# Performance work log

Measured on AMD Instinct MI355X. Metric: run time of the kernel, lower is better.

Reference implementation:

```python
import jax, jax.numpy as jnp
import numpy as np

N_HEAD = 16
ROPE_BASE = 10000.0


def _rotate_half(x):
    # interleaved rotate: (-x2, x1) pairs, matching torch stack+flatten
    x1 = x[..., ::2]
    x2 = x[..., 1::2]
    return jnp.stack((-x2, x1), axis=-1).reshape(x.shape)


def setup_inputs() -> dict:
    key = jax.random.key(0)
    ks = jax.random.split(key, 5)
    B, S, C = 4, 2048, 1024
    sc = 1.0 / np.sqrt(C)
    return {
        "x": jax.random.normal(ks[0], (B, S, C), jnp.float32),
        "W_qkv": jax.random.normal(ks[1], (C, 3 * C), jnp.float32) * sc,
        "b_qkv": jax.random.normal(ks[2], (3 * C,), jnp.float32) * 0.02,
        "W_proj": jax.random.normal(ks[3], (C, C), jnp.float32) * sc,
        "b_proj": jax.random.normal(ks[4], (C,), jnp.float32) * 0.02,
    }


def reference(x, W_qkv, b_qkv, W_proj, b_proj):
    B, S, C = x.shape
    H = N_HEAD
    D = C // H

    qkv = x @ W_qkv + b_qkv                       # [B,S,3C]
    q, k, v = jnp.split(qkv, 3, axis=-1)
    q = q.reshape(B, S, H, D).transpose(0, 2, 1, 3)  # [B,H,S,D]
    k = k.reshape(B, S, H, D).transpose(0, 2, 1, 3)
    v = v.reshape(B, S, H, D).transpose(0, 2, 1, 3)

    # RoPE cache (offset=0), faithful to source: emb = cat(freqs, freqs)
    inv_freq = 1.0 / (ROPE_BASE ** (jnp.arange(0, D, 2, dtype=jnp.float32) / D))
    pos = jnp.arange(S, dtype=jnp.float32)
    freqs = jnp.outer(pos, inv_freq)              # [S, D/2]
    emb = jnp.concatenate((freqs, freqs), axis=-1)  # [S, D]
    cos = jnp.cos(emb)[None, None, :, :]
    sin = jnp.sin(emb)[None, None, :, :]

    q = q * cos + _rotate_half(q) * sin
    k = k * cos + _rotate_half(k) * sin

    scale = 1.0 / jnp.sqrt(jnp.asarray(D, x.dtype))
    scores = jnp.einsum("bhqd,bhkd->bhqk", q, k) * scale  # [B,H,S,S]
    causal = jnp.tril(jnp.ones((S, S), dtype=bool))
    scores = jnp.where(causal[None, None], scores, jnp.asarray(-jnp.inf, x.dtype))
    att = jax.nn.softmax(scores, axis=-1)
    out = jnp.einsum("bhqk,bhkd->bhqd", att, v)    # [B,H,S,D]

    out = out.transpose(0, 2, 1, 3).reshape(B, S, C)
    out = out @ W_proj + b_proj                    # dropout=0 (eval)
    return out
```

## Files before the change

### kernel.cpp

```cpp
#include <hip/hip_runtime.h>
#include <hip/hip_bf16.h>
#include <math.h>

#define B_ 4
#define S_ 2048
#define C_ 1024
#define H_ 16
#define D_ 64
#define M_ (B_*S_)
#define NQKV (3*C_)
#define KDIM C_

typedef float f32x4 __attribute__((ext_vector_type(4)));
typedef float f32x16 __attribute__((ext_vector_type(16)));
typedef short bf16x8 __attribute__((ext_vector_type(8)));

static __device__ __forceinline__ ushort f2bf(float f){
    __hip_bfloat16 h = __float2bfloat16(f);
    union { __hip_bfloat16 b; ushort u; } v; v.b = h;
    return v.u;
}

static __device__ __forceinline__ void gload16(const ushort* g, ushort* l){
    __builtin_amdgcn_global_load_lds((__attribute__((address_space(1))) void*)g,
                                     (__attribute__((address_space(3))) void*)l,
                                     16, 0, 0);
}

__global__ void k_prep(const float* __restrict__ x, const float* __restrict__ Wqkv,
                       const float* __restrict__ Wproj,
                       ushort* __restrict__ xb, ushort* __restrict__ wqt,
                       ushort* __restrict__ wpt, unsigned* __restrict__ csT){
    __shared__ float tile[32][33];
    int blk = blockIdx.x, tid = threadIdx.x;
    if (blk < 2048){
        const int n4 = M_*KDIM/4;
        for (int i = blk*256 + tid; i < n4; i += 2048*256){
            float4 v = *(const float4*)(x + (size_t)i*4);
            ushort4 o = { f2bf(v.x), f2bf(v.y), f2bf(v.z), f2bf(v.w) };
            *(ushort4*)(xb + (size_t)i*4) = o;
        }
    } else if (blk < 5120){
        int t = blk - 2048;
        int c0 = (t % 96)*32, r0 = (t / 96)*32;
        int tx = tid & 31, ty = tid >> 5;
        for (int j = ty; j < 32; j += 8)
            tile[j][tx] = Wqkv[(size_t)(r0 + j)*NQKV + c0 + tx];
        __syncthreads();
        for (int j = ty; j < 32; j += 8)
            wqt[(size_t)(c0 + tx)*KDIM + r0 + j] = f2bf(tile[j][tx]);
    } else if (blk < 6144){
        int t = blk - 5120;
        int c0 = (t & 31)*32, r0 = (t >> 5)*32;
        int tx = tid & 31, ty = tid >> 5;
        for (int j = ty; j < 32; j += 8)
            tile[j][tx] = Wproj[(size_t)(r0 + j)*C_ + c0 + tx];
        __syncthreads();
        for (int j = ty; j < 32; j += 8)
            wpt[(size_t)(c0 + tx)*KDIM + r0 + j] = f2bf(tile[j][tx]);
    } else {
        int t = (blk - 6144)*256 + tid;
        int d = t >> 11, pos = t & 2047;
        float invf = powf(10000.0f, -(float)(d & 31) / 32.0f);
        float ang = (float)pos * invf;
        csT[t] = (unsigned)f2bf(cosf(ang)) | ((unsigned)f2bf(sinf(ang)) << 16);
    }
}

__launch_bounds__(512, 4)
__global__ void k_qkv(const ushort* __restrict__ xb, const ushort* __restrict__ wt,
                      const float* __restrict__ bqkv, const unsigned* __restrict__ csT,
                      ushort* __restrict__ qb, ushort* __restrict__ kb, ushort* __restrict__ vT){
    __shared__ __align__(16) ushort As[2][256][32];
    __shared__ __align__(16) ushort Bs[2][128][32];
    int bid = blockIdx.x;
    int lin = (bid & 7)*96 + (bid >> 3);
    int bx = lin % 24, by = lin / 24;
    int M0 = by*256, N0 = bx*128;
    int tid = threadIdx.x;
    int wid = tid >> 6, lane = tid & 63;
    int wm = wid >> 1, wn = wid & 1;
    int lrow = lane & 15, lk = lane >> 4;
    int swu = (lrow >> 1) & 3;

    int scol = (((lane & 3) ^ ((lane >> 3) & 3))) * 8;
    const ushort* gA0 = &xb[(size_t)(M0 + wid*16 + (lane >> 2))*KDIM + scol];
    const ushort* gA1 = gA0 + (size_t)128*KDIM;
    const ushort* gB0 = &wt[(size_t)(N0 + wid*16 + (lane >> 2))*KDIM + scol];

    f32x4 acc[4][4] = {};
    int cur = 0;
    gload16(gA0, &As[0][wid*16][0]);
    gload16(gA1, &As[0][128 + wid*16][0]);
    gload16(gB0, &Bs[0][wid*16][0]);
    __syncthreads();

    for (int k0 = 0; k0 < KDIM; k0 += 32){
        int nk = k0 + 32;
        if (nk < KDIM){
            gload16(gA0 + nk, &As[cur^1][wid*16][0]);
            gload16(gA1 + nk, &As[cur^1][128 + wid*16][0]);
            gload16(gB0 + nk, &Bs[cur^1][wid*16][0]);
        }
        bf16x8 a[4], b[4];
#pragma unroll
        for (int mi = 0; mi < 4; mi++)
            a[mi] = *(const bf16x8*)(&As[cur][wm*64 + mi*16 + lrow][(lk ^ swu)*8]);
#pragma unroll
        for (int ni = 0; ni < 4; ni++)
            b[ni] = *(const bf16x8*)(&Bs[cur][wn*64 + ni*16 + lrow][(lk ^ swu)*8]);
#pragma unroll
        for (int mi = 0; mi < 4; mi++)
#pragma unroll
            for (int ni = 0; ni < 4; ni++)
                acc[mi][ni] = __builtin_amdgcn_mfma_f32_16x16x32_bf16(a[mi], b[ni], acc[mi][ni], 0, 0, 0);
        __syncthreads();
        cur ^= 1;
    }
#pragma unroll
    for (int mi = 0; mi < 4; mi++)
#pragma unroll
    for (int ni = 0; ni < 4; ni++){
        int gn = N0 + wn*64 + ni*16 + lrow;
        float bias = bqkv[gn];
        int which = gn >> 10;
        int cn = gn & 1023;
        int h = cn >> 6, d = cn & 63;
        int gm0 = M0 + wm*64 + mi*16 + lk*4;
        int bb = gm0 >> 11, pos0 = gm0 & 2047;
        if (which == 2){
            ushort4 o = { f2bf(acc[mi][ni][0] + bias), f2bf(acc[mi][ni][1] + bias),
                          f2bf(acc[mi][ni][2] + bias), f2bf(acc[mi][ni][3] + bias) };
            *(ushort4*)(&vT[(((size_t)(bb*H_ + h))*D_ + d)*S_ + pos0]) = o;
        } else {
            uint4 cs4 = *(const uint4*)(&csT[d*2048 + pos0]);
            unsigned csa[4] = { cs4.x, cs4.y, cs4.z, cs4.w };
#pragma unroll
            for (int rr = 0; rr < 4; rr++){
                float val = acc[mi][ni][rr] + bias;
                float rot = __shfl_xor(val, 1);
                unsigned cs = csa[rr];
                float c = __uint_as_float(cs << 16);
                float s = __uint_as_float(cs & 0xffff0000u);
                float o = val*c + ((d & 1) ? rot : -rot)*s;
                if (which == 0) o *= 0.18033688f;
                int out_idx = (((bb*H_ + h)*S_) + pos0 + rr)*D_ + d;
                ((which == 0) ? qb : kb)[out_idx] = f2bf(o);
            }
        }
    }
}

__launch_bounds__(512, 4)
__global__ void k_proj(const ushort* __restrict__ ab, const ushort* __restrict__ wt,
                       const float* __restrict__ bias, float* __restrict__ out){
    __shared__ __align__(16) ushort As[2][256][32];
    __shared__ __align__(16) ushort Bs[2][128][32];
    int bid = blockIdx.x;
    int lin = (bid & 7)*32 + (bid >> 3);
    int bx = lin & 7, by = lin >> 3;
    int M0 = by*256, N0 = bx*128;
    int tid = threadIdx.x;
    int wid = tid >> 6, lane = tid & 63;
    int wm = wid >> 1, wn = wid & 1;
    int lrow = lane & 15, lk = lane >> 4;
    int swu = (lrow >> 1) & 3;

    int scol = (((lane & 3) ^ ((lane >> 3) & 3))) * 8;
    const ushort* gA0 = &ab[(size_t)(M0 + wid*16 + (lane >> 2))*KDIM + scol];
    const ushort* gA1 = gA0 + (size_t)128*KDIM;
    const ushort* gB0 = &wt[(size_t)(N0 + wid*16 + (lane >> 2))*KDIM + scol];

    f32x4 acc[4][4] = {};
    int cur = 0;
    gload16(gA0, &As[0][wid*16][0]);
    gload16(gA1, &As[0][128 + wid*16][0]);
    gload16(gB0, &Bs[0][wid*16][0]);
    __syncthreads();

    for (int k0 = 0; k0 < KDIM; k0 += 32){
        int nk = k0 + 32;
        if (nk < KDIM){
            gload16(gA0 + nk, &As[cur^1][wid*16][0]);
            gload16(gA1 + nk, &As[cur^1][128 + wid*16][0]);
            gload16(gB0 + nk, &Bs[cur^1][wid*16][0]);
        }
        bf16x8 a[4], b[4];
#pragma unroll
        for (int mi = 0; mi < 4; mi++)
            a[mi] = *(const bf16x8*)(&As[cur][wm*64 + mi*16 + lrow][(lk ^ swu)*8]);
#pragma unroll
        for (int ni = 0; ni < 4; ni++)
            b[ni] = *(const bf16x8*)(&Bs[cur][wn*64 + ni*16 + lrow][(lk ^ swu)*8]);
#pragma unroll
        for (int mi = 0; mi < 4; mi++)
#pragma unroll
            for (int ni = 0; ni < 4; ni++)
                acc[mi][ni] = __builtin_amdgcn_mfma_f32_16x16x32_bf16(a[mi], b[ni], acc[mi][ni], 0, 0, 0);
        __syncthreads();
        cur ^= 1;
    }
#pragma unroll
    for (int mi = 0; mi < 4; mi++)
#pragma unroll
    for (int ni = 0; ni < 4; ni++){
        int gn = N0 + wn*64 + ni*16 + lrow;
        float bv = bias[gn];
#pragma unroll
        for (int rr = 0; rr < 4; rr++){
            int gm = M0 + wm*64 + mi*16 + lk*4 + rr;
            out[(size_t)gm*C_ + gn] = acc[mi][ni][rr] + bv;
        }
    }
}

__launch_bounds__(256, 3)
__global__ void k_attn(const ushort* __restrict__ qb, const ushort* __restrict__ kb,
                       const ushort* __restrict__ vT, ushort* __restrict__ ob){
    __shared__ __align__(16) ushort Ks[64][64];
    __shared__ __align__(16) ushort Vs[64][64];
    int bh = blockIdx.x;
    int qt = (gridDim.y - 1) - blockIdx.y;
    int bb = bh >> 4, h = bh & 15;
    int tid = threadIdx.x, wid = tid >> 6, lane = tid & 63;
    int lq = lane & 31, hi = lane >> 5;
    const ushort* qp = qb + (size_t)bh*S_*D_;
    const ushort* kp = kb + (size_t)bh*S_*D_;
    const ushort* vp = vT + (size_t)bh*D_*S_;
    int qw = qt*128 + wid*32;
    int qrow = qw + lq;
    int swz = lq & 7;

    bf16x8 fq[4];
#pragma unroll
    for (int c = 0; c < 4; c++)
        fq[c] = *(const bf16x8*)(&qp[qrow*D_ + c*16 + hi*8]);

    f32x16 acc0 = {}, acc1 = {};
    float m = -1e30f, l = 0.0f;

    int tr = tid >> 3, tcu = tid & 7;
    int twu = (tcu ^ (tr & 7)) * 8;
    int tc = tcu * 8;

    int4 ra = *(const int4*)(&kp[tr*D_ + tc]);
    int4 rb = *(const int4*)(&kp[(tr+32)*D_ + tc]);
    int4 rc = *(const int4*)(&vp[(size_t)tr*S_ + tc]);
    int4 rd = *(const int4*)(&vp[(size_t)(tr+32)*S_ + tc]);

    int nit = 2*qt + 2;
    for (int it = 0; it < nit; ++it){
        int j0 = it*64;
        *(int4*)(&Ks[tr][twu])    = ra;
        *(int4*)(&Ks[tr+32][twu]) = rb;
        *(int4*)(&Vs[tr][twu])    = rc;
        *(int4*)(&Vs[tr+32][twu]) = rd;
        __syncthreads();
        if (it + 1 < nit){
            int j1 = j0 + 64;
            ra = *(const int4*)(&kp[(j1+tr)*D_ + tc]);
            rb = *(const int4*)(&kp[(j1+tr+32)*D_ + tc]);
            rc = *(const int4*)(&vp[(size_t)tr*S_ + j1 + tc]);
            rd = *(const int4*)(&vp[(size_t)(tr+32)*S_ + j1 + tc]);
        }
        int rel = qw - j0;
        if (rel >= 0){
            bool diag0 = (rel == 0);
            bool have1 = (rel >= 32);
            bool diag1 = (rel == 32);
            f32x16 z0 = {}, z1 = {};
            __builtin_amdgcn_s_setprio(1);
#pragma unroll
            for (int c = 0; c < 4; c++){
                bf16x8 kf = *(const bf16x8*)(&Ks[lq][((2*c + hi) ^ swz)*8]);
                z0 = __builtin_amdgcn_mfma_f32_32x32x16_bf16(kf, fq[c], z0, 0, 0, 0);
            }
            if (have1){
#pragma unroll
                for (int c = 0; c < 4; c++){
                    bf16x8 kf = *(const bf16x8*)(&Ks[32 + lq][((2*c + hi) ^ swz)*8]);
                    z1 = __builtin_amdgcn_mfma_f32_32x32x16_bf16(kf, fq[c], z1, 0, 0, 0);
                }
            }
            __builtin_amdgcn_s_setprio(0);
            if (diag0){
#pragma unroll
                for (int r = 0; r < 16; r++)
                    if (((r & 3) + 8*(r >> 2) + 4*hi) > lq) z0[r] = -1e30f;
            }
            if (diag1){
#pragma unroll
                for (int r = 0; r < 16; r++)
                    if (((r & 3) + 8*(r >> 2) + 4*hi) > lq) z1[r] = -1e30f;
            }
            float tmax = z0[0];
#pragma unroll
            for (int r = 1; r < 16; r++) tmax = fmaxf(tmax, z0[r]);
            if (have1){
#pragma unroll
                for (int r = 0; r < 16; r++) tmax = fmaxf(tmax, z1[r]);
            }
            tmax = fmaxf(tmax, __shfl_xor(tmax, 32));
            if (__any(tmax > m)){
                float newm = fmaxf(m, tmax);
                float resc = exp2f(m - newm);
                m = newm; l *= resc;
#pragma unroll
                for (int r = 0; r < 16; r++){ acc0[r] *= resc; acc1[r] *= resc; }
            }
            float rsum = 0.0f;
#pragma unroll
            for (int r = 0; r < 16; r++){ z0[r] = exp2f(z0[r] - m); rsum += z0[r]; }
            if (have1){
#pragma unroll
                for (int r = 0; r < 16; r++){ z1[r] = exp2f(z1[r] - m); rsum += z1[r]; }
            }
            rsum += __shfl_xor(rsum, 32);
            l += rsum;

#define PV_SUB(zz, r0_, su, t) do {                                              \
    unsigned w0, w1, w2, w3;                                                     \
    asm("v_cvt_pk_bf16_f32 %0, %1, %2" : "=v"(w0) : "v"(zz[r0_+0]), "v"(zz[r0_+1])); \
    asm("v_cvt_pk_bf16_f32 %0, %1, %2" : "=v"(w1) : "v"(zz[r0_+2]), "v"(zz[r0_+3])); \
    asm("v_cvt_pk_bf16_f32 %0, %1, %2" : "=v"(w2) : "v"(zz[r0_+4]), "v"(zz[r0_+5])); \
    asm("v_cvt_pk_bf16_f32 %0, %1, %2" : "=v"(w3) : "v"(zz[r0_+6]), "v"(zz[r0_+7])); \
    auto s02 = __builtin_amdgcn_permlane32_swap(w0, w2, false, false);            \
    auto s13 = __builtin_amdgcn_permlane32_swap(w1, w3, false, false);            \
    union { unsigned u[4]; bf16x8 v; } pf;                                       \
    pf.u[0] = s02[0]; pf.u[1] = s13[0]; pf.u[2] = s02[1]; pf.u[3] = s13[1];      \
    bf16x8 vf0 = *(const bf16x8*)(&Vs[lq][(((su)*4 + (t)*2 + hi) ^ swz)*8]);     \
    acc0 = __builtin_amdgcn_mfma_f32_32x32x16_bf16(vf0, pf.v, acc0, 0, 0, 0);    \
    bf16x8 vf1 = *(const bf16x8*)(&Vs[32 + lq][(((su)*4 + (t)*2 + hi) ^ swz)*8]);\
    acc1 = __builtin_amdgcn_mfma_f32_32x32x16_bf16(vf1, pf.v, acc1, 0, 0, 0);    \
} while(0)

            __builtin_amdgcn_s_setprio(1);
            PV_SUB(z0, 0, 0, 0);
            PV_SUB(z0, 8, 0, 1);
            if (have1){
                PV_SUB(z1, 0, 1, 0);
                PV_SUB(z1, 8, 1, 1);
            }
            __builtin_amdgcn_s_setprio(0);
#undef PV_SUB
        }
        __syncthreads();
    }
    float rl = 1.0f / l;
#pragma unroll
    for (int rg = 0; rg < 4; rg++){
        ushort4 o0 = { f2bf(acc0[rg*4+0]*rl), f2bf(acc0[rg*4+1]*rl),
                       f2bf(acc0[rg*4+2]*rl), f2bf(acc0[rg*4+3]*rl) };
        *(ushort4*)(&ob[((size_t)(bb*S_ + qrow))*C_ + h*D_ + rg*8 + hi*4]) = o0;
        ushort4 o1 = { f2bf(acc1[rg*4+0]*rl), f2bf(acc1[rg*4+1]*rl),
                       f2bf(acc1[rg*4+2]*rl), f2bf(acc1[rg*4+3]*rl) };
        *(ushort4*)(&ob[((size_t)(bb*S_ + qrow))*C_ + h*D_ + 32 + rg*8 + hi*4]) = o1;
    }
}

extern "C" void kernel_launch(void* const* d_in, const int* in_sizes, int n_in,
                              void* d_out, int out_size, void* d_ws, size_t ws_size,
                              hipStream_t stream) {
    const float* x     = (const float*)d_in[0];
    const float* Wqkv  = (const float*)d_in[1];
    const float* bqkv  = (const float*)d_in[2];
    const float* Wproj = (const float*)d_in[3];
    const float* bproj = (const float*)d_in[4];
    float* out = (float*)d_out;

    char* ws = (char*)d_ws;
    ushort*   xb   = (ushort*)(ws);
    ushort*   wqt  = (ushort*)(ws + (16u<<20));
    ushort*   wpt  = (ushort*)(ws + (22u<<20));
    unsigned* csT  = (unsigned*)(ws + (24u<<20));
    ushort*   qbuf = (ushort*)(ws + (25u<<20));
    ushort*   kbuf = (ushort*)(ws + (41u<<20));
    ushort*   vbuf = (ushort*)(ws + (57u<<20));
    ushort*   obuf = (ushort*)(ws + (73u<<20));

    k_prep<<<6656, 256, 0, stream>>>(x, Wqkv, Wproj, xb, wqt, wpt, csT);
    k_qkv<<<768, 512, 0, stream>>>(xb, wqt, bqkv, csT, qbuf, kbuf, vbuf);
    k_attn<<<dim3(B_*H_, S_/128), 256, 0, stream>>>(qbuf, kbuf, vbuf, obuf);
    k_proj<<<256, 512, 0, stream>>>(obuf, wpt, bproj, out);
}
```

Before: 190.4 us.

## Widen attention blocks to 256 queries, lazy softmax rescale, transpose RoPE table

```diff
diff --git a/kernel.cpp b/kernel.cpp
--- a/kernel.cpp
+++ b/kernel.cpp
@@ -60,7 +60,7 @@
             wpt[(size_t)(c0 + tx)*KDIM + r0 + j] = f2bf(tile[j][tx]);
     } else {
         int t = (blk - 6144)*256 + tid;
-        int d = t >> 11, pos = t & 2047;
+        int pos = t >> 6, d = t & 63;
         float invf = powf(10000.0f, -(float)(d & 31) / 32.0f);
         float ang = (float)pos * invf;
         csT[t] = (unsigned)f2bf(cosf(ang)) | ((unsigned)f2bf(sinf(ang)) << 16);
@@ -133,13 +133,11 @@
                           f2bf(acc[mi][ni][2] + bias), f2bf(acc[mi][ni][3] + bias) };
             *(ushort4*)(&vT[(((size_t)(bb*H_ + h))*D_ + d)*S_ + pos0]) = o;
         } else {
-            uint4 cs4 = *(const uint4*)(&csT[d*2048 + pos0]);
-            unsigned csa[4] = { cs4.x, cs4.y, cs4.z, cs4.w };
 #pragma unroll
             for (int rr = 0; rr < 4; rr++){
                 float val = acc[mi][ni][rr] + bias;
                 float rot = __shfl_xor(val, 1);
-                unsigned cs = csa[rr];
+                unsigned cs = csT[(pos0 + rr)*64 + d];
                 float c = __uint_as_float(cs << 16);
                 float s = __uint_as_float(cs & 0xffff0000u);
                 float o = val*c + ((d & 1) ? rot : -rot)*s;
@@ -214,7 +212,7 @@
     }
 }
 
-__launch_bounds__(256, 3)
+__launch_bounds__(512, 2)
 __global__ void k_attn(const ushort* __restrict__ qb, const ushort* __restrict__ kb,
                        const ushort* __restrict__ vT, ushort* __restrict__ ob){
     __shared__ __align__(16) ushort Ks[64][64];
@@ -227,7 +225,7 @@
     const ushort* qp = qb + (size_t)bh*S_*D_;
     const ushort* kp = kb + (size_t)bh*S_*D_;
     const ushort* vp = vT + (size_t)bh*D_*S_;
-    int qw = qt*128 + wid*32;
+    int qw = qt*256 + wid*32;
     int qrow = qw + lq;
     int swz = lq & 7;
 
@@ -239,29 +237,23 @@
     f32x16 acc0 = {}, acc1 = {};
     float m = -1e30f, l = 0.0f;
 
-    int tr = tid >> 3, tcu = tid & 7;
-    int twu = (tcu ^ (tr & 7)) * 8;
-    int tc = tcu * 8;
-
-    int4 ra = *(const int4*)(&kp[tr*D_ + tc]);
-    int4 rb = *(const int4*)(&kp[(tr+32)*D_ + tc]);
-    int4 rc = *(const int4*)(&vp[(size_t)tr*S_ + tc]);
-    int4 rd = *(const int4*)(&vp[(size_t)(tr+32)*S_ + tc]);
-
-    int nit = 2*qt + 2;
+    int sr = tid >> 3, su = tid & 7;
+    int swr = (su ^ (sr & 7)) * 8;
+    int sc = su * 8;
+
+    int4 ra = *(const int4*)(&kp[sr*D_ + sc]);
+    int4 rc = *(const int4*)(&vp[(size_t)sr*S_ + sc]);
+
+    int nit = 4*qt + 4;
     for (int it = 0; it < nit; ++it){
         int j0 = it*64;
-        *(int4*)(&Ks[tr][twu])    = ra;
-        *(int4*)(&Ks[tr+32][twu]) = rb;
-        *(int4*)(&Vs[tr][twu])    = rc;
-        *(int4*)(&Vs[tr+32][twu]) = rd;
+        *(int4*)(&Ks[sr][swr]) = ra;
+        *(int4*)(&Vs[sr][swr]) = rc;
         __syncthreads();
         if (it + 1 < nit){
             int j1 = j0 + 64;
-            ra = *(const int4*)(&kp[(j1+tr)*D_ + tc]);
-            rb = *(const int4*)(&kp[(j1+tr+32)*D_ + tc]);
-            rc = *(const int4*)(&vp[(size_t)tr*S_ + j1 + tc]);
-            rd = *(const int4*)(&vp[(size_t)(tr+32)*S_ + j1 + tc]);
+            ra = *(const int4*)(&kp[(j1+sr)*D_ + sc]);
+            rc = *(const int4*)(&vp[(size_t)sr*S_ + j1 + sc]);
         }
         int rel = qw - j0;
         if (rel >= 0){
@@ -301,7 +293,7 @@
                 for (int r = 0; r < 16; r++) tmax = fmaxf(tmax, z1[r]);
             }
             tmax = fmaxf(tmax, __shfl_xor(tmax, 32));
-            if (__any(tmax > m)){
+            if (!__all(tmax <= m + 8.0f)){
                 float newm = fmaxf(m, tmax);
                 float resc = exp2f(m - newm);
                 m = newm; l *= resc;
@@ -318,20 +310,20 @@
             rsum += __shfl_xor(rsum, 32);
             l += rsum;
 
-#define PV_SUB(zz, r0_, su, t) do {                                              \
-    unsigned w0, w1, w2, w3;                                                     \
+#define PV_SUB(zz, r0_, su_, t_) do {                                             \
+    unsigned w0, w1, w2, w3;                                                      \
     asm("v_cvt_pk_bf16_f32 %0, %1, %2" : "=v"(w0) : "v"(zz[r0_+0]), "v"(zz[r0_+1])); \
     asm("v_cvt_pk_bf16_f32 %0, %1, %2" : "=v"(w1) : "v"(zz[r0_+2]), "v"(zz[r0_+3])); \
     asm("v_cvt_pk_bf16_f32 %0, %1, %2" : "=v"(w2) : "v"(zz[r0_+4]), "v"(zz[r0_+5])); \
     asm("v_cvt_pk_bf16_f32 %0, %1, %2" : "=v"(w3) : "v"(zz[r0_+6]), "v"(zz[r0_+7])); \
-    auto s02 = __builtin_amdgcn_permlane32_swap(w0, w2, false, false);            \
-    auto s13 = __builtin_amdgcn_permlane32_swap(w1, w3, false, false);            \
-    union { unsigned u[4]; bf16x8 v; } pf;                                       \
-    pf.u[0] = s02[0]; pf.u[1] = s13[0]; pf.u[2] = s02[1]; pf.u[3] = s13[1];      \
-    bf16x8 vf0 = *(const bf16x8*)(&Vs[lq][(((su)*4 + (t)*2 + hi) ^ swz)*8]);     \
-    acc0 = __builtin_amdgcn_mfma_f32_32x32x16_bf16(vf0, pf.v, acc0, 0, 0, 0);    \
-    bf16x8 vf1 = *(const bf16x8*)(&Vs[32 + lq][(((su)*4 + (t)*2 + hi) ^ swz)*8]);\
-    acc1 = __builtin_amdgcn_mfma_f32_32x32x16_bf16(vf1, pf.v, acc1, 0, 0, 0);    \
+    auto s02 = __builtin_amdgcn_permlane32_swap(w0, w2, false, false);             \
+    auto s13 = __builtin_amdgcn_permlane32_swap(w1, w3, false, false);             \
+    union { unsigned u[4]; bf16x8 v; } pf;                                        \
+    pf.u[0] = s02[0]; pf.u[1] = s13[0]; pf.u[2] = s02[1]; pf.u[3] = s13[1];       \
+    bf16x8 vf0 = *(const bf16x8*)(&Vs[lq][(((su_)*4 + (t_)*2 + hi) ^ swz)*8]);    \
+    acc0 = __builtin_amdgcn_mfma_f32_32x32x16_bf16(vf0, pf.v, acc0, 0, 0, 0);     \
+    bf16x8 vf1 = *(const bf16x8*)(&Vs[32 + lq][(((su_)*4 + (t_)*2 + hi) ^ swz)*8]);\
+    acc1 = __builtin_amdgcn_mfma_f32_32x32x16_bf16(vf1, pf.v, acc1, 0, 0, 0);     \
 } while(0)
 
             __builtin_amdgcn_s_setprio(1);
@@ -380,6 +372,6 @@
 
     k_prep<<<6656, 256, 0, stream>>>(x, Wqkv, Wproj, xb, wqt, wpt, csT);
     k_qkv<<<768, 512, 0, stream>>>(xb, wqt, bqkv, csT, qbuf, kbuf, vbuf);
-    k_attn<<<dim3(B_*H_, S_/128), 256, 0, stream>>>(qbuf, kbuf, vbuf, obuf);
+    k_attn<<<dim3(B_*H_, S_/256), 512, 0, stream>>>(qbuf, kbuf, vbuf, obuf);
     k_proj<<<256, 512, 0, stream>>>(obuf, wpt, bproj, out);
 }
```

After: 186.5 us. 2.1% less time.
